# Optimization experiments

Hardware: AMD Instinct MI355X
Metric: run time of the kernel (lower is better)

The kernel has to match this reference:

```python
import jax, jax.numpy as jnp
import numpy as np

K = 8192
C = 512
BETA = 0.25
DECAY = 0.99
EPS = 1e-05


def setup_inputs() -> dict:
    key = jax.random.key(0)
    k1, k2, k3 = jax.random.split(key, 3)
    z_e = jax.random.normal(k1, (8, 1024, C), dtype=jnp.float32)
    codebook = jax.random.normal(k2, (K, C), dtype=jnp.float32) * 0.02
    cluster_size = jax.random.uniform(k3, (K,), dtype=jnp.float32)
    embed_avg = codebook  # buffer initialized as a copy of the codebook
    return {"z_e": z_e, "codebook": codebook, "cluster_size": cluster_size, "embed_avg": embed_avg}


def reference(z_e, codebook, cluster_size, embed_avg):
    B, N, Cc = z_e.shape
    z = z_e.reshape(-1, Cc)            # [T, C]
    z32 = z.astype(jnp.float32)
    cw = codebook.astype(jnp.float32)  # [K, C]

    # squared L2 distances: ||z||^2 - 2 z.e + ||e||^2  -> [T, K]
    dist = (jnp.sum(z32 * z32, axis=1, keepdims=True)
            - 2.0 * (z32 @ cw.T)
            + jnp.sum(cw * cw, axis=1)[None, :])
    idx = jnp.argmin(dist, axis=1)     # [T]
    z_q = cw[idx]                      # [T, C] gather

    vq_loss = BETA * jnp.mean((z32 - jax.lax.stop_gradient(z_q)) ** 2)

    # straight-through estimator
    z_st = z + jax.lax.stop_gradient(z_q.astype(z.dtype) - z)
    z_q_st = z_st.reshape(B, N, Cc)
    indices = idx.reshape(B, N)

    # EMA codebook update (training path; no_grad in original)
    counts = jax.ops.segment_sum(jnp.ones(idx.shape, jnp.float32), idx, num_segments=K)
    embed_sum = jax.ops.segment_sum(z32, idx, num_segments=K)  # [K, C] scatter-add
    new_cluster_size = cluster_size * DECAY + counts * (1.0 - DECAY)
    new_embed_avg = embed_avg * DECAY + embed_sum * (1.0 - DECAY)
    n = jnp.maximum(jnp.sum(new_cluster_size), 1.0)
    smoothed = (new_cluster_size + EPS) / (n + K * EPS) * n
    new_codebook = new_embed_avg / smoothed[:, None]

    return z_q_st, indices, vq_loss, new_codebook, new_cluster_size, new_embed_avg
```

## Files before the change

### kernel.cpp

```cpp
#include <hip/hip_runtime.h>
#include <cstdint>
#include <cstddef>

#define T_TOK 8192
#define K_CODE 8192
#define C_DIM 512
#define BETA 0.25f
#define DECAY 0.99f
#define ONE_MINUS_DECAY 0.01f
#define EPS_F 1e-5f
#define K_EPS 0.08192f
#define MARGIN 0.0625f

#define ZQ_OFF   ((size_t)0)
#define IDX_OFF  ((size_t)4194304)
#define LOSS_OFF ((size_t)4202496)
#define NCB_OFF  ((size_t)4202497)
#define NCS_OFF  ((size_t)8396801)
#define NEA_OFF  ((size_t)8404993)

#define CP_F_OFF    ((size_t)2097152)
#define SLAB1_F_OFF ((size_t)8404994)
#define SLAB2_F_OFF ((size_t)(8404994 + 524288))
#define LOSSP_F_OFF ((size_t)9453570)
#define LIST_I_OFF  ((size_t)10502146)
#define OFFSB_I_OFF ((size_t)10518530)

#define WS_ZNORM  0
#define WS_ENORM  8192
#define WS_ICOUNT 16384
#define WS_NSUM   24576

typedef _Float16 half8 __attribute__((ext_vector_type(8)));
typedef _Float16 half4v __attribute__((ext_vector_type(4)));
typedef float floatx4 __attribute__((ext_vector_type(4)));
typedef unsigned long long ull;

__device__ __forceinline__ void gload16(const void* g, void* l) {
    __builtin_amdgcn_global_load_lds(
        (const __attribute__((address_space(1))) void*)g,
        (__attribute__((address_space(3))) void*)l, 16, 0, 0);
}

__device__ __forceinline__ unsigned umin32(unsigned a, unsigned b) { return a < b ? a : b; }
__device__ __forceinline__ unsigned umax32(unsigned a, unsigned b) { return a > b ? a : b; }

__device__ __forceinline__ float dot8(float4 z0, float4 z1, float4 c0, float4 c1) {
    float p = 0.0f;
    p = fmaf(z0.x, c0.x, p); p = fmaf(z0.y, c0.y, p);
    p = fmaf(z0.z, c0.z, p); p = fmaf(z0.w, c0.w, p);
    p = fmaf(z1.x, c1.x, p); p = fmaf(z1.y, c1.y, p);
    p = fmaf(z1.z, c1.z, p); p = fmaf(z1.w, c1.w, p);
    return p;
}

__global__ __launch_bounds__(256) void prep_kernel(const float* __restrict__ z,
                                                   const float* __restrict__ cb,
                                                   _Float16* __restrict__ zp,
                                                   _Float16* __restrict__ cp,
                                                   float* __restrict__ ws) {
    int tid = threadIdx.x;
    int row = blockIdx.x * 2 + (tid >> 7);
    int l128 = tid & 127;
    const float* src;
    _Float16* dst;
    float* nrm;
    if (row < T_TOK) { src = z + (size_t)row * C_DIM; dst = zp + (size_t)row * C_DIM; nrm = ws + WS_ZNORM + row; }
    else { int r = row - T_TOK; src = cb + (size_t)r * C_DIM; dst = cp + (size_t)r * C_DIM; nrm = ws + WS_ENORM + r; }
    float4 v = *(const float4*)(src + l128 * 4);
    half4v h;
    h[0] = (_Float16)v.x; h[1] = (_Float16)v.y;
    h[2] = (_Float16)v.z; h[3] = (_Float16)v.w;
    *(half4v*)(dst + l128 * 4) = h;
    float s = v.x * v.x + v.y * v.y + v.z * v.z + v.w * v.w;
    #pragma unroll
    for (int m = 32; m; m >>= 1) s += __shfl_down(s, m, 64);
    __shared__ float red[4];
    if ((tid & 63) == 0) red[tid >> 6] = s;
    __syncthreads();
    if ((tid & 127) == 0) nrm[0] = red[tid >> 6] + red[(tid >> 6) + 1];
}

__global__ __launch_bounds__(256) void dist_mfma_kernel(
        const _Float16* __restrict__ zp, const _Float16* __restrict__ cp,
        const float* __restrict__ znorm, const float* __restrict__ enorm,
        unsigned* __restrict__ slab1, unsigned* __restrict__ slab2) {
    __shared__ __align__(16) _Float16 As[128 * 32];
    __shared__ __align__(16) _Float16 Bs[128 * 32];
    __shared__ unsigned red2[128][2][2];
    const int tid = threadIdx.x;
    const int w = tid >> 6, lane = tid & 63;
    const int quad = lane >> 4, lr = lane & 15;
    const int wm = w >> 1, wn = w & 1;

    const int GRID_N = 64, GROUP_M = 16;
    int pid0 = blockIdx.x;
    int pid = (pid0 & 7) * 512 + (pid0 >> 3);
    int per = GROUP_M * GRID_N;
    int g = pid / per;
    int local = pid % per;
    int bm = g * GROUP_M + (local & (GROUP_M - 1));
    int bn = local / GROUP_M;
    const int mBase = bm * 128, nBase = bn * 128;

    int r0 = (w * 2 + 0) * 16 + (lane >> 2);
    int r1 = (w * 2 + 1) * 16 + (lane >> 2);
    int cq = (((lane & 3) ^ ((lane >> 3) & 3))) * 8;
    const _Float16* ga0 = zp + (size_t)(mBase + r0) * C_DIM + cq;
    const _Float16* ga1 = zp + (size_t)(mBase + r1) * C_DIM + cq;
    const _Float16* gb0 = cp + (size_t)(nBase + r0) * C_DIM + cq;
    const _Float16* gb1 = cp + (size_t)(nBase + r1) * C_DIM + cq;
    _Float16* la0 = As + (w * 2 + 0) * 512;
    _Float16* la1 = As + (w * 2 + 1) * 512;
    _Float16* lb0 = Bs + (w * 2 + 0) * 512;
    _Float16* lb1 = Bs + (w * 2 + 1) * 512;

    const int slotA = (quad ^ ((lr >> 1) & 3)) * 8;
    const _Float16* aFrag = As + ((size_t)(wm * 64 + lr)) * 32 + slotA;
    const _Float16* bFrag = Bs + ((size_t)(wn * 64 + lr)) * 32 + slotA;

    floatx4 acc[4][4] = {};

    for (int it = 0; it < 16; ++it) {
        __syncthreads();
        gload16(ga0, la0);
        gload16(ga1, la1);
        gload16(gb0, lb0);
        gload16(gb1, lb1);
        ga0 += 32; ga1 += 32; gb0 += 32; gb1 += 32;
        __syncthreads();
        half8 af[4], bf[4];
        #pragma unroll
        for (int i = 0; i < 4; ++i) af[i] = *(const half8*)(aFrag + i * 16 * 32);
        #pragma unroll
        for (int j = 0; j < 4; ++j) bf[j] = *(const half8*)(bFrag + j * 16 * 32);
        #pragma unroll
        for (int i = 0; i < 4; ++i)
            #pragma unroll
            for (int j = 0; j < 4; ++j)
                acc[i][j] = __builtin_amdgcn_mfma_f32_16x16x32_f16(af[i], bf[j], acc[i][j], 0, 0, 0);
    }

    float en[4];
    #pragma unroll
    for (int j = 0; j < 4; ++j) en[j] = enorm[nBase + wn * 64 + j * 16 + lr];
    #pragma unroll
    for (int i = 0; i < 4; ++i) {
        #pragma unroll
        for (int r = 0; r < 4; ++r) {
            int lrow = wm * 64 + i * 16 + quad * 4 + r;
            float zn = znorm[mBase + lrow];
            unsigned t1 = 0xFFFFFFFFu, t2 = 0xFFFFFFFFu;
            #pragma unroll
            for (int j = 0; j < 4; ++j) {
                int nLoc = wn * 64 + j * 16 + lr;
                float s = (zn - 2.0f * acc[i][j][r]) + en[j];
                s = fmaxf(s, 0.0f);
                unsigned key = ((__float_as_uint(s) + 0x40u) & 0xFFFFFF80u) | (unsigned)nLoc;
                if (key < t1) { t2 = t1; t1 = key; } else if (key < t2) t2 = key;
            }
            #pragma unroll
            for (int msk = 1; msk < 16; msk <<= 1) {
                unsigned o1 = (unsigned)__shfl_xor((int)t1, msk, 64);
                unsigned o2 = (unsigned)__shfl_xor((int)t2, msk, 64);
                unsigned n1 = umin32(t1, o1);
                unsigned n2 = umin32(umax32(t1, o1), umin32(t2, o2));
                t1 = n1; t2 = n2;
            }
            if (lr == 0) { red2[lrow][wn][0] = t1; red2[lrow][wn][1] = t2; }
        }
    }
    __syncthreads();
    if (tid < 128) {
        unsigned a1 = red2[tid][0][0], a2 = red2[tid][0][1];
        unsigned b1 = red2[tid][1][0], b2 = red2[tid][1][1];
        unsigned m1 = umin32(a1, b1);
        unsigned m2 = umin32(umax32(a1, b1), umin32(a2, b2));
        slab1[(size_t)(mBase + tid) * 64 + bn] = m1;
        slab2[(size_t)(mBase + tid) * 64 + bn] = m2;
    }
}

__global__ __launch_bounds__(256) void refine_gather_kernel(
        const float* __restrict__ z, const float* __restrict__ cb,
        const float* __restrict__ znorm, const float* __restrict__ enorm,
        const unsigned* __restrict__ slab1, const unsigned* __restrict__ slab2,
        float* __restrict__ out, int* __restrict__ icount,
        float* __restrict__ lossP) {
    int tid = threadIdx.x;
    int wv = tid >> 6, lane = tid & 63;
    int t = blockIdx.x * 4 + wv;

    unsigned s1 = slab1[(size_t)t * 64 + lane];
    unsigned s2 = slab2[(size_t)t * 64 + lane];
    const float* zr = z + (size_t)t * C_DIM + lane * 8;
    float4 z0 = *(const float4*)zr;
    float4 z1 = *(const float4*)(zr + 4);

    unsigned v = s1;
    #pragma unroll
    for (int m = 32; m; m >>= 1) v = umin32(v, (unsigned)__shfl_xor((int)v, m, 64));
    float thr = __uint_as_float(v & 0xFFFFFF80u) + MARGIN;
    float d1 = __uint_as_float(s1 & 0xFFFFFF80u);
    float d2 = __uint_as_float(s2 & 0xFFFFFF80u);
    bool full = d2 < thr;
    ull fullMask = __ballot(full);
    ull singleMask = __ballot(!full && d1 < thr);

    float zn = znorm[t];
    ull lbest = ~0ull;

    while (fullMask) {
        int bn = __builtin_ctzll(fullMask);
        fullMask &= fullMask - 1;
        int nb = bn * 128;
        for (int rep = 0; rep < 32; ++rep) {
            int n0 = nb + rep * 4;
            const float* cr0 = cb + (size_t)(n0    ) * C_DIM + lane * 8;
            const float* cr1 = cb + (size_t)(n0 + 1) * C_DIM + lane * 8;
            const float* cr2 = cb + (size_t)(n0 + 2) * C_DIM + lane * 8;
            const float* cr3 = cb + (size_t)(n0 + 3) * C_DIM + lane * 8;
            float4 c00 = *(const float4*)cr0, c01 = *(const float4*)(cr0 + 4);
            float4 c10 = *(const float4*)cr1, c11 = *(const float4*)(cr1 + 4);
            float4 c20 = *(const float4*)cr2, c21 = *(const float4*)(cr2 + 4);
            float4 c30 = *(const float4*)cr3, c31 = *(const float4*)(cr3 + 4);
            float p0 = dot8(z0, z1, c00, c01);
            float p1 = dot8(z0, z1, c10, c11);
            float p2 = dot8(z0, z1, c20, c21);
            float p3 = dot8(z0, z1, c30, c31);
            #pragma unroll
            for (int m = 32; m; m >>= 1) {
                p0 += __shfl_xor(p0, m, 64);
                p1 += __shfl_xor(p1, m, 64);
                p2 += __shfl_xor(p2, m, 64);
                p3 += __shfl_xor(p3, m, 64);
            }
            float s0 = (zn - 2.0f * p0) + enorm[n0];
            float s1f = (zn - 2.0f * p1) + enorm[n0 + 1];
            float s2f = (zn - 2.0f * p2) + enorm[n0 + 2];
            float s3f = (zn - 2.0f * p3) + enorm[n0 + 3];
            ull k0 = ((ull)__float_as_uint(s0) << 32) | (unsigned)(n0);
            ull k1 = ((ull)__float_as_uint(s1f) << 32) | (unsigned)(n0 + 1);
            ull k2 = ((ull)__float_as_uint(s2f) << 32) | (unsigned)(n0 + 2);
            ull k3 = ((ull)__float_as_uint(s3f) << 32) | (unsigned)(n0 + 3);
            ull kk = k0 < k1 ? k0 : k1;
            ull kl = k2 < k3 ? k2 : k3;
            kk = kk < kl ? kk : kl;
            lbest = lbest < kk ? lbest : kk;
        }
    }
    while (singleMask) {
        int bn = __builtin_ctzll(singleMask);
        singleMask &= singleMask - 1;
        int n = bn * 128 + (__shfl((int)s1, bn, 64) & 0x7F);
        const float* cr = cb + (size_t)n * C_DIM + lane * 8;
        float4 c0 = *(const float4*)cr;
        float4 c1 = *(const float4*)(cr + 4);
        float p = dot8(z0, z1, c0, c1);
        #pragma unroll
        for (int m = 32; m; m >>= 1) p += __shfl_xor(p, m, 64);
        float s = (zn - 2.0f * p) + enorm[n];
        ull pk = ((ull)__float_as_uint(s) << 32) | (unsigned)n;
        lbest = lbest < pk ? lbest : pk;
    }
    int idx = (int)(unsigned)(lbest & 0xFFFFFFFFull);

    const float* qr = cb + (size_t)idx * C_DIM + lane * 8;
    float4 q0 = *(const float4*)qr;
    float4 q1 = *(const float4*)(qr + 4);
    float4 o0, o1;
    o0.x = z0.x + (q0.x - z0.x); o0.y = z0.y + (q0.y - z0.y);
    o0.z = z0.z + (q0.z - z0.z); o0.w = z0.w + (q0.w - z0.w);
    o1.x = z1.x + (q1.x - z1.x); o1.y = z1.y + (q1.y - z1.y);
    o1.z = z1.z + (q1.z - z1.z); o1.w = z1.w + (q1.w - z1.w);
    float* zq = out + ZQ_OFF + (size_t)t * C_DIM + lane * 8;
    *(float4*)zq = o0;
    *(float4*)(zq + 4) = o1;
    float d, l = 0.0f;
    d = z0.x - q0.x; l = fmaf(d, d, l);
    d = z0.y - q0.y; l = fmaf(d, d, l);
    d = z0.z - q0.z; l = fmaf(d, d, l);
    d = z0.w - q0.w; l = fmaf(d, d, l);
    d = z1.x - q1.x; l = fmaf(d, d, l);
    d = z1.y - q1.y; l = fmaf(d, d, l);
    d = z1.z - q1.z; l = fmaf(d, d, l);
    d = z1.w - q1.w; l = fmaf(d, d, l);
    #pragma unroll
    for (int m = 32; m; m >>= 1) l += __shfl_down(l, m, 64);
    if (lane == 0) {
        lossP[t] = l * (BETA / ((float)T_TOK * (float)C_DIM));
        out[IDX_OFF + t] = (float)idx;
        atomicAdd(&icount[idx], 1);
    }
}

__global__ __launch_bounds__(256) void scan_ncs_scatter_kernel(
        const int* __restrict__ icount, const float* __restrict__ cs,
        const float* __restrict__ lossP, const float* __restrict__ outIdx,
        int* __restrict__ offsB, int* __restrict__ list,
        float* __restrict__ out, float* __restrict__ nsum) {
    __shared__ int tot[256];
    __shared__ int ofs[8192];
    int tid = threadIdx.x;
    int v[32];
    int s = 0;
    float ncsSum = 0.0f, lsum = 0.0f;
    #pragma unroll
    for (int j = 0; j < 32; ++j) {
        int k = tid * 32 + j;
        int x = icount[k];
        v[j] = s;
        s += x;
        float ncs = cs[k] * DECAY + (float)x * ONE_MINUS_DECAY;
        out[NCS_OFF + k] = ncs;
        ncsSum += ncs;
        lsum += lossP[k];
    }
    tot[tid] = s;
    __syncthreads();
    for (int d = 1; d < 256; d <<= 1) {
        int x = (tid >= d) ? tot[tid - d] : 0;
        __syncthreads();
        tot[tid] += x;
        __syncthreads();
    }
    int excl = tid ? tot[tid - 1] : 0;
    #pragma unroll
    for (int j = 0; j < 32; ++j) {
        int k = tid * 32 + j;
        int o = excl + v[j];
        ofs[k] = o;
        offsB[k] = o;
    }
    __syncthreads();
    for (int base = 0; base < T_TOK; base += 256) {
        int t = base + tid;
        int idx = (int)outIdx[t];
        int slot = atomicAdd(&ofs[idx], 1);
        list[slot] = t;
    }
    float a = ncsSum, l = lsum;
    #pragma unroll
    for (int m = 32; m; m >>= 1) { a += __shfl_down(a, m, 64); l += __shfl_down(l, m, 64); }
    __shared__ float redA[4], redL[4];
    if ((tid & 63) == 0) { redA[tid >> 6] = a; redL[tid >> 6] = l; }
    __syncthreads();
    if (tid == 0) {
        nsum[0] = (redA[0] + redA[1]) + (redA[2] + redA[3]);
        out[LOSS_OFF] = (redL[0] + redL[1]) + (redL[2] + redL[3]);
    }
}

__global__ __launch_bounds__(256) void percode_sum_kernel(
        const float* __restrict__ z, const int* __restrict__ list,
        const int* __restrict__ offsB, const int* __restrict__ icount,
        float* __restrict__ out) {
    int k = blockIdx.x;
    int tid = threadIdx.x;
    int off = offsB[k], cnt = icount[k];
    float a0 = 0.0f, a1 = 0.0f;
    for (int i = 0; i < cnt; ++i) {
        int t = list[off + i];
        const float* zrow = z + (size_t)t * C_DIM;
        a0 += zrow[tid];
        a1 += zrow[tid + 256];
    }
    out[NCB_OFF + (size_t)k * C_DIM + tid] = a0;
    out[NCB_OFF + (size_t)k * C_DIM + tid + 256] = a1;
}

__global__ __launch_bounds__(256) void finalize_kernel(const float* __restrict__ ea,
                                                       float* __restrict__ out,
                                                       const float* __restrict__ nsumP) {
    int k = blockIdx.x;
    int tid = threadIdx.x;
    float n = fmaxf(*nsumP, 1.0f);
    float ncs = out[NCS_OFF + k];
    float smoothed = ((ncs + EPS_F) / (n + K_EPS)) * n;
    #pragma unroll
    for (int s = 0; s < 2; ++s) {
        int c = tid + s * 256;
        size_t o = (size_t)k * C_DIM + c;
        float es = out[NCB_OFF + o];
        float nea = ea[o] * DECAY + es * ONE_MINUS_DECAY;
        out[NEA_OFF + o] = nea;
        out[NCB_OFF + o] = nea / smoothed;
    }
}

extern "C" void kernel_launch(void* const* d_in, const int* in_sizes, int n_in,
                              void* d_out, int out_size, void* d_ws, size_t ws_size,
                              hipStream_t stream) {
    const float* z  = (const float*)d_in[0];
    const float* cb = (const float*)d_in[1];
    const float* cs = (const float*)d_in[2];
    const float* ea = (const float*)d_in[3];
    float* out = (float*)d_out;
    float* ws  = (float*)d_ws;
    _Float16* zp = (_Float16*)out;
    _Float16* cp = (_Float16*)(out + CP_F_OFF);
    float* lossP = out + LOSSP_F_OFF;
    unsigned* slab1 = (unsigned*)(out + SLAB1_F_OFF);
    unsigned* slab2 = (unsigned*)(out + SLAB2_F_OFF);
    int* list  = (int*)(out + LIST_I_OFF);
    int* offsB = (int*)(out + OFFSB_I_OFF);
    int* icount = (int*)(ws + WS_ICOUNT);
    float* nsum = ws + WS_NSUM;

    hipMemsetAsync(ws + WS_ICOUNT, 0, (size_t)8192 * 4, stream);

    prep_kernel<<<8192, 256, 0, stream>>>(z, cb, zp, cp, ws);
    dist_mfma_kernel<<<4096, 256, 0, stream>>>(zp, cp, ws + WS_ZNORM, ws + WS_ENORM, slab1, slab2);
    refine_gather_kernel<<<2048, 256, 0, stream>>>(z, cb, ws + WS_ZNORM, ws + WS_ENORM,
                                                   slab1, slab2, out, icount, lossP);
    scan_ncs_scatter_kernel<<<1, 256, 0, stream>>>(icount, cs, lossP, out + IDX_OFF,
                                                   offsB, list, out, nsum);
    percode_sum_kernel<<<8192, 256, 0, stream>>>(z, list, offsB, icount, out);
    finalize_kernel<<<8192, 256, 0, stream>>>(ea, out, nsum);
}
```

Baseline: 275.2 us.

## Fuse per-code sum with finalize, fold memset into prep, split refine wave into groups

The per-code embed-sum and EMA finalize kernels are merged into one kernel, so the intermediate sums are not written to and re-read from the output buffer. This path runs only when the workspace is large enough to hold the list and offsets. The icount memset is folded into prep_kernel, removing a separate launch. In the refine kernel each wavefront now evaluates four codes at once using 16-lane groups, which shortens the shuffle reductions and handles up to four single-candidate blocks per iteration, at the cost of extra registers holding z in a second layout.

After: 262.6 us. -4.6%, faster.

```diff
diff --git a/kernel.cpp b/kernel.cpp
--- a/kernel.cpp
+++ b/kernel.cpp
@@ -30,6 +30,9 @@
 #define WS_ENORM  8192
 #define WS_ICOUNT 16384
 #define WS_NSUM   24576
+#define WS_LIST   24608
+#define WS_OFFSB  32800
+#define WS_NEED_BYTES ((size_t)(32800 + 8192) * 4)
 
 typedef _Float16 half8 __attribute__((ext_vector_type(8)));
 typedef _Float16 half4v __attribute__((ext_vector_type(4)));
@@ -44,6 +47,15 @@
 
 __device__ __forceinline__ unsigned umin32(unsigned a, unsigned b) { return a < b ? a : b; }
 __device__ __forceinline__ unsigned umax32(unsigned a, unsigned b) { return a > b ? a : b; }
+__device__ __forceinline__ ull umin64(ull a, ull b) { return a < b ? a : b; }
+
+__device__ inline ull shfl_xor_u64(ull v, int m) {
+    int lo = (int)(unsigned)(v & 0xFFFFFFFFull);
+    int hi = (int)(unsigned)(v >> 32);
+    lo = __shfl_xor(lo, m, 64);
+    hi = __shfl_xor(hi, m, 64);
+    return ((ull)(unsigned)hi << 32) | (unsigned)lo;
+}
 
 __device__ __forceinline__ float dot8(float4 z0, float4 z1, float4 c0, float4 c1) {
     float p = 0.0f;
@@ -58,8 +70,10 @@
                                                    const float* __restrict__ cb,
                                                    _Float16* __restrict__ zp,
                                                    _Float16* __restrict__ cp,
-                                                   float* __restrict__ ws) {
-    int tid = threadIdx.x;
+                                                   float* __restrict__ ws,
+                                                   int* __restrict__ icount) {
+    int tid = threadIdx.x;
+    if (blockIdx.x < 32) icount[blockIdx.x * 256 + tid] = 0;
     int row = blockIdx.x * 2 + (tid >> 7);
     int l128 = tid & 127;
     const float* src;
@@ -189,13 +203,20 @@
         float* __restrict__ lossP) {
     int tid = threadIdx.x;
     int wv = tid >> 6, lane = tid & 63;
+    int grp = lane >> 4, gl = lane & 15;
     int t = blockIdx.x * 4 + wv;
 
     unsigned s1 = slab1[(size_t)t * 64 + lane];
     unsigned s2 = slab2[(size_t)t * 64 + lane];
-    const float* zr = z + (size_t)t * C_DIM + lane * 8;
-    float4 z0 = *(const float4*)zr;
-    float4 z1 = *(const float4*)(zr + 4);
+    const float* zr = z + (size_t)t * C_DIM;
+    float4 z0 = *(const float4*)(zr + lane * 8);
+    float4 z1 = *(const float4*)(zr + lane * 8 + 4);
+    float4 zca[4], zcb[4];
+    #pragma unroll
+    for (int c = 0; c < 4; ++c) {
+        zca[c] = *(const float4*)(zr + c * 128 + gl * 8);
+        zcb[c] = *(const float4*)(zr + c * 128 + gl * 8 + 4);
+    }
 
     unsigned v = s1;
     #pragma unroll
@@ -215,53 +236,69 @@
         fullMask &= fullMask - 1;
         int nb = bn * 128;
         for (int rep = 0; rep < 32; ++rep) {
-            int n0 = nb + rep * 4;
-            const float* cr0 = cb + (size_t)(n0    ) * C_DIM + lane * 8;
-            const float* cr1 = cb + (size_t)(n0 + 1) * C_DIM + lane * 8;
-            const float* cr2 = cb + (size_t)(n0 + 2) * C_DIM + lane * 8;
-            const float* cr3 = cb + (size_t)(n0 + 3) * C_DIM + lane * 8;
-            float4 c00 = *(const float4*)cr0, c01 = *(const float4*)(cr0 + 4);
-            float4 c10 = *(const float4*)cr1, c11 = *(const float4*)(cr1 + 4);
-            float4 c20 = *(const float4*)cr2, c21 = *(const float4*)(cr2 + 4);
-            float4 c30 = *(const float4*)cr3, c31 = *(const float4*)(cr3 + 4);
-            float p0 = dot8(z0, z1, c00, c01);
-            float p1 = dot8(z0, z1, c10, c11);
-            float p2 = dot8(z0, z1, c20, c21);
-            float p3 = dot8(z0, z1, c30, c31);
+            int n = nb + rep * 4 + grp;
+            const float* cr = cb + (size_t)n * C_DIM + gl * 8;
+            float4 ca0 = *(const float4*)(cr);
+            float4 cb0 = *(const float4*)(cr + 4);
+            float4 ca1 = *(const float4*)(cr + 128);
+            float4 cb1 = *(const float4*)(cr + 132);
+            float4 ca2 = *(const float4*)(cr + 256);
+            float4 cb2 = *(const float4*)(cr + 260);
+            float4 ca3 = *(const float4*)(cr + 384);
+            float4 cb3 = *(const float4*)(cr + 388);
+            float pA = dot8(zca[0], zcb[0], ca0, cb0);
+            float pB = dot8(zca[1], zcb[1], ca1, cb1);
+            float pC = dot8(zca[2], zcb[2], ca2, cb2);
+            float pD = dot8(zca[3], zcb[3], ca3, cb3);
+            float p = (pA + pB) + (pC + pD);
             #pragma unroll
-            for (int m = 32; m; m >>= 1) {
-                p0 += __shfl_xor(p0, m, 64);
-                p1 += __shfl_xor(p1, m, 64);
-                p2 += __shfl_xor(p2, m, 64);
-                p3 += __shfl_xor(p3, m, 64);
+            for (int m = 1; m <= 8; m <<= 1) p += __shfl_xor(p, m, 64);
+            float s = (zn - 2.0f * p) + enorm[n];
+            ull pk = ((ull)__float_as_uint(s) << 32) | (unsigned)n;
+            pk = umin64(pk, shfl_xor_u64(pk, 16));
+            pk = umin64(pk, shfl_xor_u64(pk, 32));
+            lbest = umin64(lbest, pk);
+        }
+    }
+    while (singleMask) {
+        ull m2 = singleMask;
+        int myb = -1;
+        #pragma unroll
+        for (int j = 0; j < 4; ++j) {
+            if (m2) {
+                int b = __builtin_ctzll(m2);
+                m2 &= m2 - 1;
+                if (j == grp) myb = b;
             }
-            float s0 = (zn - 2.0f * p0) + enorm[n0];
-            float s1f = (zn - 2.0f * p1) + enorm[n0 + 1];
-            float s2f = (zn - 2.0f * p2) + enorm[n0 + 2];
-            float s3f = (zn - 2.0f * p3) + enorm[n0 + 3];
-            ull k0 = ((ull)__float_as_uint(s0) << 32) | (unsigned)(n0);
-            ull k1 = ((ull)__float_as_uint(s1f) << 32) | (unsigned)(n0 + 1);
-            ull k2 = ((ull)__float_as_uint(s2f) << 32) | (unsigned)(n0 + 2);
-            ull k3 = ((ull)__float_as_uint(s3f) << 32) | (unsigned)(n0 + 3);
-            ull kk = k0 < k1 ? k0 : k1;
-            ull kl = k2 < k3 ? k2 : k3;
-            kk = kk < kl ? kk : kl;
-            lbest = lbest < kk ? lbest : kk;
         }
-    }
-    while (singleMask) {
-        int bn = __builtin_ctzll(singleMask);
-        singleMask &= singleMask - 1;
-        int n = bn * 128 + (__shfl((int)s1, bn, 64) & 0x7F);
-        const float* cr = cb + (size_t)n * C_DIM + lane * 8;
-        float4 c0 = *(const float4*)cr;
-        float4 c1 = *(const float4*)(cr + 4);
-        float p = dot8(z0, z1, c0, c1);
-        #pragma unroll
-        for (int m = 32; m; m >>= 1) p += __shfl_xor(p, m, 64);
-        float s = (zn - 2.0f * p) + enorm[n];
-        ull pk = ((ull)__float_as_uint(s) << 32) | (unsigned)n;
-        lbest = lbest < pk ? lbest : pk;
+        singleMask = m2;
+        int bsrc = (myb >= 0) ? myb : 0;
+        int scode = __shfl((int)s1, bsrc, 64) & 0x7F;
+        ull pk = ~0ull;
+        if (myb >= 0) {
+            int n = myb * 128 + scode;
+            const float* cr = cb + (size_t)n * C_DIM + gl * 8;
+            float4 ca0 = *(const float4*)(cr);
+            float4 cb0 = *(const float4*)(cr + 4);
+            float4 ca1 = *(const float4*)(cr + 128);
+            float4 cb1 = *(const float4*)(cr + 132);
+            float4 ca2 = *(const float4*)(cr + 256);
+            float4 cb2 = *(const float4*)(cr + 260);
+            float4 ca3 = *(const float4*)(cr + 384);
+            float4 cb3 = *(const float4*)(cr + 388);
+            float pA = dot8(zca[0], zcb[0], ca0, cb0);
+            float pB = dot8(zca[1], zcb[1], ca1, cb1);
+            float pC = dot8(zca[2], zcb[2], ca2, cb2);
+            float pD = dot8(zca[3], zcb[3], ca3, cb3);
+            float p = (pA + pB) + (pC + pD);
+            #pragma unroll
+            for (int m = 1; m <= 8; m <<= 1) p += __shfl_xor(p, m, 64);
+            float s = (zn - 2.0f * p) + enorm[n];
+            pk = ((ull)__float_as_uint(s) << 32) | (unsigned)n;
+        }
+        pk = umin64(pk, shfl_xor_u64(pk, 16));
+        pk = umin64(pk, shfl_xor_u64(pk, 32));
+        lbest = umin64(lbest, pk);
     }
     int idx = (int)(unsigned)(lbest & 0xFFFFFFFFull);
 
@@ -351,6 +388,34 @@
     }
 }
 
+__global__ __launch_bounds__(256) void percode_finalize_kernel(
+        const float* __restrict__ z, const float* __restrict__ ea,
+        const int* __restrict__ list, const int* __restrict__ offsB,
+        const int* __restrict__ icount, float* __restrict__ out,
+        const float* __restrict__ nsumP) {
+    int k = blockIdx.x;
+    int tid = threadIdx.x;
+    int off = offsB[k], cnt = icount[k];
+    float a0 = 0.0f, a1 = 0.0f;
+    for (int i = 0; i < cnt; ++i) {
+        int t = list[off + i];
+        const float* zrow = z + (size_t)t * C_DIM;
+        a0 += zrow[tid];
+        a1 += zrow[tid + 256];
+    }
+    float n = fmaxf(*nsumP, 1.0f);
+    float ncs = out[NCS_OFF + k];
+    float smoothed = ((ncs + EPS_F) / (n + K_EPS)) * n;
+    size_t o0 = (size_t)k * C_DIM + tid;
+    size_t o1 = o0 + 256;
+    float nea0 = ea[o0] * DECAY + a0 * ONE_MINUS_DECAY;
+    float nea1 = ea[o1] * DECAY + a1 * ONE_MINUS_DECAY;
+    out[NEA_OFF + o0] = nea0;
+    out[NEA_OFF + o1] = nea1;
+    out[NCB_OFF + o0] = nea0 / smoothed;
+    out[NCB_OFF + o1] = nea1 / smoothed;
+}
+
 __global__ __launch_bounds__(256) void percode_sum_kernel(
         const float* __restrict__ z, const int* __restrict__ list,
         const int* __restrict__ offsB, const int* __restrict__ icount,
@@ -402,19 +467,23 @@
     float* lossP = out + LOSSP_F_OFF;
     unsigned* slab1 = (unsigned*)(out + SLAB1_F_OFF);
     unsigned* slab2 = (unsigned*)(out + SLAB2_F_OFF);
-    int* list  = (int*)(out + LIST_I_OFF);
-    int* offsB = (int*)(out + OFFSB_I_OFF);
     int* icount = (int*)(ws + WS_ICOUNT);
     float* nsum = ws + WS_NSUM;
 
-    hipMemsetAsync(ws + WS_ICOUNT, 0, (size_t)8192 * 4, stream);
-
-    prep_kernel<<<8192, 256, 0, stream>>>(z, cb, zp, cp, ws);
+    bool wsbig = ws_size >= WS_NEED_BYTES;
+    int* list  = wsbig ? (int*)(ws + WS_LIST)  : (int*)(out + LIST_I_OFF);
+    int* offsB = wsbig ? (int*)(ws + WS_OFFSB) : (int*)(out + OFFSB_I_OFF);
+
+    prep_kernel<<<8192, 256, 0, stream>>>(z, cb, zp, cp, ws, icount);
     dist_mfma_kernel<<<4096, 256, 0, stream>>>(zp, cp, ws + WS_ZNORM, ws + WS_ENORM, slab1, slab2);
     refine_gather_kernel<<<2048, 256, 0, stream>>>(z, cb, ws + WS_ZNORM, ws + WS_ENORM,
                                                    slab1, slab2, out, icount, lossP);
     scan_ncs_scatter_kernel<<<1, 256, 0, stream>>>(icount, cs, lossP, out + IDX_OFF,
                                                    offsB, list, out, nsum);
-    percode_sum_kernel<<<8192, 256, 0, stream>>>(z, list, offsB, icount, out);
-    finalize_kernel<<<8192, 256, 0, stream>>>(ea, out, nsum);
-}
+    if (wsbig) {
+        percode_finalize_kernel<<<8192, 256, 0, stream>>>(z, ea, list, offsB, icount, out, nsum);
+    } else {
+        percode_sum_kernel<<<8192, 256, 0, stream>>>(z, list, offsB, icount, out);
+        finalize_kernel<<<8192, 256, 0, stream>>>(ea, out, nsum);
+    }
+}
```
